# Kernel tuning notes

Hardware: AMD Instinct MI355X
Metric: run time of the kernel (lower is better)

Reference implementation:

```python
import jax, jax.numpy as jnp
import numpy as np
from jax import lax

B, H, V, T = 64, 1024, 16384, 64


def setup_inputs() -> dict:
    key = jax.random.key(0)
    ks = jax.random.split(key, 8)
    s = 1.0 / np.sqrt(H)
    return {
        "encoder_hidden": jax.random.normal(ks[0], (B, H), jnp.float32),
        "encoder_cell": jax.random.normal(ks[1], (B, H), jnp.float32),
        "W_ih": jax.random.normal(ks[2], (4 * H, H), jnp.float32) * s,
        "W_hh": jax.random.normal(ks[3], (4 * H, H), jnp.float32) * s,
        "b_ih": jnp.zeros((4 * H,), jnp.float32),
        "b_hh": jnp.zeros((4 * H,), jnp.float32),
        "W_out": jax.random.normal(ks[4], (V, H), jnp.float32) * s,
        "b_out": jnp.zeros((V,), jnp.float32),
        "embedding": jax.random.normal(ks[5], (V, H), jnp.float32),
        "init_input": jnp.zeros((1, H), jnp.float32),
        "max_len": T,
        "eos_idx": 0,
    }


def reference(encoder_hidden, encoder_cell, W_ih, W_hh, b_ih, b_hh,
              W_out, b_out, embedding, init_input, max_len, eos_idx):
    batch, hidden = encoder_hidden.shape
    vocab = W_out.shape[0]
    x0 = jnp.broadcast_to(init_input, (batch, hidden))
    mask0 = jnp.ones((1, batch), dtype=encoder_hidden.dtype)

    def step(carry, _):
        h, c, x, mask = carry
        # torch.nn.LSTMCell gate math
        gates = x @ W_ih.T + b_ih + h @ W_hh.T + b_hh  # [B, 4H]
        i, f, g, o = jnp.split(gates, 4, axis=-1)
        i = jax.nn.sigmoid(i)
        f = jax.nn.sigmoid(f)
        g = jnp.tanh(g)
        o = jax.nn.sigmoid(o)
        c_new = f * c + i * g
        h_new = o * jnp.tanh(c_new)
        logit = h_new @ W_out.T + b_out  # [B, V]
        # eval-mode path: hard argmax one-hot
        predict = jax.nn.one_hot(jnp.argmax(logit, axis=1), vocab, dtype=mask.dtype)
        mask_new = mask * (1.0 - predict[:, eos_idx])  # [1, B]
        x_next = predict @ embedding  # [B, H]
        return (h_new, c_new, x_next, mask_new), (predict, logit, mask)

    carry0 = (encoder_hidden, encoder_cell, x0, mask0)
    _, (predicts, logits, masks) = lax.scan(step, carry0, None, length=max_len)
    # predicts/logits: [T, B, V]; masks: [T, 1, B]
    return predicts, logits, masks
```

## Files before the change

### kernel.cpp

```cpp
#include <hip/hip_runtime.h>
#include <math.h>

#define B 64
#define H 1024
#define V 16384
#define T 64
constexpr int KT = 32;
constexpr size_t TBV = (size_t)T * B * V;

__global__ __launch_bounds__(256) void k_init(
    const float* __restrict__ enc_h, const float* __restrict__ enc_c,
    const float* __restrict__ init_input,
    float* __restrict__ h, float* __restrict__ c,
    float* __restrict__ x, float* __restrict__ mask)
{
    int i = blockIdx.x * 256 + threadIdx.x;
    if (i < B * H) {
        h[i] = enc_h[i];
        c[i] = enc_c[i];
        x[i] = init_input[i & (H - 1)];
    }
    if (i < B) mask[i] = 1.0f;
}

__global__ __launch_bounds__(256) void k_gates(
    const float* __restrict__ x, const float* __restrict__ h,
    const float* __restrict__ W_ih, const float* __restrict__ W_hh,
    float* __restrict__ gpart)
{
    const int nt   = blockIdx.x >> 3;
    const int ks   = blockIdx.x & 7;
    const int pair = ks >> 2;
    const int kbase = (ks & 3) * 256;
    const float* __restrict__ A = pair ? h : x;
    const float* __restrict__ W = pair ? W_hh : W_ih;

    __shared__ __align__(16) float a_lds[KT][68];
    __shared__ __align__(16) float w_lds[KT][68];

    const int tid = threadIdx.x;
    const int tb = tid >> 4;
    const int tn = tid & 15;
    float acc[4][4];
#pragma unroll
    for (int i = 0; i < 4; ++i)
#pragma unroll
        for (int j = 0; j < 4; ++j) acc[i][j] = 0.f;

    const int kk = tid & 31;
    const int r  = tid >> 5;

    for (int kc = 0; kc < 256 / KT; ++kc) {
        const int k0 = kbase + kc * KT;
#pragma unroll
        for (int j = 0; j < 8; ++j) {
            int row = r * 8 + j;
            a_lds[kk][row] = A[row * H + k0 + kk];
            w_lds[kk][row] = W[(nt * 64 + row) * H + k0 + kk];
        }
        __syncthreads();
#pragma unroll
        for (int k2 = 0; k2 < KT; ++k2) {
            float4 av = *(const float4*)&a_lds[k2][tb * 4];
            float4 wv = *(const float4*)&w_lds[k2][tn * 4];
            acc[0][0] = fmaf(av.x, wv.x, acc[0][0]);
            acc[0][1] = fmaf(av.x, wv.y, acc[0][1]);
            acc[0][2] = fmaf(av.x, wv.z, acc[0][2]);
            acc[0][3] = fmaf(av.x, wv.w, acc[0][3]);
            acc[1][0] = fmaf(av.y, wv.x, acc[1][0]);
            acc[1][1] = fmaf(av.y, wv.y, acc[1][1]);
            acc[1][2] = fmaf(av.y, wv.z, acc[1][2]);
            acc[1][3] = fmaf(av.y, wv.w, acc[1][3]);
            acc[2][0] = fmaf(av.z, wv.x, acc[2][0]);
            acc[2][1] = fmaf(av.z, wv.y, acc[2][1]);
            acc[2][2] = fmaf(av.z, wv.z, acc[2][2]);
            acc[2][3] = fmaf(av.z, wv.w, acc[2][3]);
            acc[3][0] = fmaf(av.w, wv.x, acc[3][0]);
            acc[3][1] = fmaf(av.w, wv.y, acc[3][1]);
            acc[3][2] = fmaf(av.w, wv.z, acc[3][2]);
            acc[3][3] = fmaf(av.w, wv.w, acc[3][3]);
        }
        __syncthreads();
    }

    float* outp = gpart + (size_t)ks * B * 4096;
#pragma unroll
    for (int i = 0; i < 4; ++i) {
        float4 v = make_float4(acc[i][0], acc[i][1], acc[i][2], acc[i][3]);
        *(float4*)&outp[(size_t)(tb * 4 + i) * 4096 + nt * 64 + tn * 4] = v;
    }
}

__global__ __launch_bounds__(256) void k_lstm(
    const float* __restrict__ gpart,
    const float* __restrict__ b_ih, const float* __restrict__ b_hh,
    float* __restrict__ h, float* __restrict__ c)
{
    int idx = blockIdx.x * 256 + threadIdx.x;
    int b = idx >> 10, j = idx & 1023;
    float s[4];
#pragma unroll
    for (int g = 0; g < 4; ++g) {
        int m = g * H + j;
        float v = b_ih[m] + b_hh[m];
#pragma unroll
        for (int ksp = 0; ksp < 8; ++ksp)
            v += gpart[(size_t)ksp * B * 4096 + (size_t)b * 4096 + m];
        s[g] = v;
    }
    float ig = 1.f / (1.f + expf(-s[0]));
    float fg = 1.f / (1.f + expf(-s[1]));
    float gg = tanhf(s[2]);
    float og = 1.f / (1.f + expf(-s[3]));
    float cn = fg * c[idx] + ig * gg;
    float hn = og * tanhf(cn);
    c[idx] = cn;
    h[idx] = hn;
}

__global__ __launch_bounds__(256) void k_logits(
    const float* __restrict__ h, const float* __restrict__ W_out,
    float* __restrict__ out0, float* __restrict__ lpart)
{
    const int nt = blockIdx.x >> 1;
    const int ks = blockIdx.x & 1;
    const int kbase = ks * 512;
    float* __restrict__ dst = ks ? lpart : out0;

    __shared__ __align__(16) float a_lds[KT][68];
    __shared__ __align__(16) float w_lds[KT][68];

    const int tid = threadIdx.x;
    const int tb = tid >> 4;
    const int tn = tid & 15;
    float acc[4][4];
#pragma unroll
    for (int i = 0; i < 4; ++i)
#pragma unroll
        for (int j = 0; j < 4; ++j) acc[i][j] = 0.f;

    const int kk = tid & 31;
    const int r  = tid >> 5;

    for (int kc = 0; kc < 512 / KT; ++kc) {
        const int k0 = kbase + kc * KT;
#pragma unroll
        for (int j = 0; j < 8; ++j) {
            int row = r * 8 + j;
            a_lds[kk][row] = h[row * H + k0 + kk];
            w_lds[kk][row] = W_out[(size_t)(nt * 64 + row) * H + k0 + kk];
        }
        __syncthreads();
#pragma unroll
        for (int k2 = 0; k2 < KT; ++k2) {
            float4 av = *(const float4*)&a_lds[k2][tb * 4];
            float4 wv = *(const float4*)&w_lds[k2][tn * 4];
            acc[0][0] = fmaf(av.x, wv.x, acc[0][0]);
            acc[0][1] = fmaf(av.x, wv.y, acc[0][1]);
            acc[0][2] = fmaf(av.x, wv.z, acc[0][2]);
            acc[0][3] = fmaf(av.x, wv.w, acc[0][3]);
            acc[1][0] = fmaf(av.y, wv.x, acc[1][0]);
            acc[1][1] = fmaf(av.y, wv.y, acc[1][1]);
            acc[1][2] = fmaf(av.y, wv.z, acc[1][2]);
            acc[1][3] = fmaf(av.y, wv.w, acc[1][3]);
            acc[2][0] = fmaf(av.z, wv.x, acc[2][0]);
            acc[2][1] = fmaf(av.z, wv.y, acc[2][1]);
            acc[2][2] = fmaf(av.z, wv.z, acc[2][2]);
            acc[2][3] = fmaf(av.z, wv.w, acc[2][3]);
            acc[3][0] = fmaf(av.w, wv.x, acc[3][0]);
            acc[3][1] = fmaf(av.w, wv.y, acc[3][1]);
            acc[3][2] = fmaf(av.w, wv.z, acc[3][2]);
            acc[3][3] = fmaf(av.w, wv.w, acc[3][3]);
        }
        __syncthreads();
    }

#pragma unroll
    for (int i = 0; i < 4; ++i) {
        float4 v = make_float4(acc[i][0], acc[i][1], acc[i][2], acc[i][3]);
        *(float4*)&dst[(size_t)(tb * 4 + i) * V + nt * 64 + tn * 4] = v;
    }
}

__global__ __launch_bounds__(256) void k_argmax(
    float* __restrict__ logit_t,
    const float* __restrict__ lpart,
    const float* __restrict__ b_out,
    const float* __restrict__ embedding,
    const int* __restrict__ eos_ptr,
    float* __restrict__ mask,
    float* __restrict__ x,
    float* __restrict__ predicts_t,
    float* __restrict__ masks_t)
{
    const int b = blockIdx.x, tid = threadIdx.x;
    __shared__ float sval[256];
    __shared__ int   sidx[256];

    float best = -INFINITY;
    int bi = 0;
    for (int v = tid; v < V; v += 256) {
        size_t off = (size_t)b * V + v;
        float val = logit_t[off] + lpart[off] + b_out[v];
        logit_t[off] = val;
        if (val > best) { best = val; bi = v; }
    }
    sval[tid] = best; sidx[tid] = bi;
    __syncthreads();
    for (int s = 128; s > 0; s >>= 1) {
        if (tid < s) {
            float v2 = sval[tid + s]; int i2 = sidx[tid + s];
            if (v2 > sval[tid] || (v2 == sval[tid] && i2 < sidx[tid])) {
                sval[tid] = v2; sidx[tid] = i2;
            }
        }
        __syncthreads();
    }
    int idx = sidx[0];
    if (tid == 0) {
        predicts_t[(size_t)b * V + idx] = 1.0f;
        float mb = mask[b];
        masks_t[b] = mb;
        if (idx == *eos_ptr) mask[b] = 0.0f;
    }
    const float4* emb4 = (const float4*)(embedding + (size_t)idx * H);
    float4* x4 = (float4*)(x + (size_t)b * H);
    for (int k = tid; k < H / 4; k += 256) x4[k] = emb4[k];
}

extern "C" void kernel_launch(void* const* d_in, const int* in_sizes, int n_in,
                              void* d_out, int out_size, void* d_ws, size_t ws_size,
                              hipStream_t stream)
{
    (void)in_sizes; (void)n_in; (void)out_size; (void)ws_size;

    const float* enc_h = (const float*)d_in[0];
    const float* enc_c = (const float*)d_in[1];
    const float* W_ih  = (const float*)d_in[2];
    const float* W_hh  = (const float*)d_in[3];
    const float* b_ih  = (const float*)d_in[4];
    const float* b_hh  = (const float*)d_in[5];
    const float* W_out = (const float*)d_in[6];
    const float* b_out = (const float*)d_in[7];
    const float* emb   = (const float*)d_in[8];
    const float* init_input = (const float*)d_in[9];
    const int* eos_ptr = (const int*)d_in[11];

    float* out = (float*)d_out;
    float* ws  = (float*)d_ws;
    float* h     = ws;
    float* c     = h + B * H;
    float* x     = c + B * H;
    float* mask  = x + B * H;
    float* gpart = mask + 64;
    float* lpart = gpart + 8 * B * 4096;

    hipMemsetAsync(d_out, 0, TBV * sizeof(float), stream);
    k_init<<<256, 256, 0, stream>>>(enc_h, enc_c, init_input, h, c, x, mask);

    for (int t = 0; t < T; ++t) {
        float* predicts_t = out + (size_t)t * B * V;
        float* logits_t   = out + TBV + (size_t)t * B * V;
        float* masks_t    = out + 2 * TBV + (size_t)t * B;

        k_gates<<<512, 256, 0, stream>>>(x, h, W_ih, W_hh, gpart);
        k_lstm<<<256, 256, 0, stream>>>(gpart, b_ih, b_hh, h, c);
        k_logits<<<512, 256, 0, stream>>>(h, W_out, logits_t, lpart);
        k_argmax<<<64, 256, 0, stream>>>(logits_t, lpart, b_out, emb, eos_ptr,
                                         mask, x, predicts_t, masks_t);
    }
}
```

Measured before the change: 5.254 ms.

## Use split-bf16 MFMA GEMMs for gates and logits with packed activations

Replaces the scalar FP32 FMA GEMMs for the LSTM gates and output logits with bf16 MFMA 32x32x16 kernels. Precision is kept near FP32 by splitting each operand into hi and lo bf16 parts and accumulating three products. Activations h and x are stored pre-split in a k-blocked layout so the MFMA A fragments load directly, while weights are converted on the fly into double-buffered LDS. The gates split-K drops from 8 partials to 2, which leaves only 64 blocks in that launch. The hi/lo split may still perturb argmax ties.

```diff
diff --git a/kernel.cpp b/kernel.cpp
--- a/kernel.cpp
+++ b/kernel.cpp
@@ -5,108 +5,141 @@
 #define H 1024
 #define V 16384
 #define T 64
-constexpr int KT = 32;
 constexpr size_t TBV = (size_t)T * B * V;
 
-__global__ __launch_bounds__(256) void k_init(
-    const float* __restrict__ enc_h, const float* __restrict__ enc_c,
-    const float* __restrict__ init_input,
-    float* __restrict__ h, float* __restrict__ c,
-    float* __restrict__ x, float* __restrict__ mask)
-{
-    int i = blockIdx.x * 256 + threadIdx.x;
-    if (i < B * H) {
-        h[i] = enc_h[i];
-        c[i] = enc_c[i];
-        x[i] = init_input[i & (H - 1)];
-    }
-    if (i < B) mask[i] = 1.0f;
-}
-
-__global__ __launch_bounds__(256) void k_gates(
-    const float* __restrict__ x, const float* __restrict__ h,
+typedef __attribute__((ext_vector_type(8))) short bhalf8;
+typedef __attribute__((ext_vector_type(16))) float f32x16;
+
+__device__ __forceinline__ void split_trunc(float a, unsigned short& hi, unsigned short& lo) {
+    unsigned u = __float_as_uint(a);
+    hi = (unsigned short)(u >> 16);
+    float hif = __uint_as_float(u & 0xFFFF0000u);
+    lo = (unsigned short)(__float_as_uint(a - hif) >> 16);
+}
+
+__device__ __forceinline__ void cvt8(const float* f, int4& hv, int4& lv) {
+    unsigned h[8], l[8];
+#pragma unroll
+    for (int j = 0; j < 8; ++j) {
+        unsigned u = __float_as_uint(f[j]);
+        h[j] = u >> 16;
+        float hif = __uint_as_float(u & 0xFFFF0000u);
+        l[j] = __float_as_uint(f[j] - hif) >> 16;
+    }
+    hv = make_int4((int)(h[0] | (h[1] << 16)), (int)(h[2] | (h[3] << 16)),
+                   (int)(h[4] | (h[5] << 16)), (int)(h[6] | (h[7] << 16)));
+    lv = make_int4((int)(l[0] | (l[1] << 16)), (int)(l[2] | (l[3] << 16)),
+                   (int)(l[4] | (l[5] << 16)), (int)(l[6] | (l[7] << 16)));
+}
+
+__device__ __forceinline__ void gemm_body(
+    const unsigned short* __restrict__ Ahi, const unsigned short* __restrict__ Alo,
+    const float* __restrict__ W, int k0, int nChunks,
+    float* __restrict__ dst, size_t dstride, int n0,
+    short (&sBh)[2][128][72], short (&sBl)[2][128][72])
+{
+    const int tid  = threadIdx.x;
+    const int wave = tid >> 6;
+    const int lane = tid & 63;
+    const int lrow = lane & 31;
+    const int lhalf = lane >> 5;
+
+    f32x16 acc0, acc1;
+#pragma unroll
+    for (int i = 0; i < 16; ++i) { acc0[i] = 0.f; acc1[i] = 0.f; }
+
+    const int r  = tid >> 1;
+    const int kh = (tid & 1) * 32;
+
+    {
+        const float* wr = W + (size_t)(n0 + r) * H + k0 + kh;
+        float f[32];
+#pragma unroll
+        for (int i = 0; i < 32; i += 4) *(float4*)&f[i] = *(const float4*)&wr[i];
+#pragma unroll
+        for (int i = 0; i < 32; i += 8) {
+            int4 hv, lv; cvt8(&f[i], hv, lv);
+            *(int4*)&sBh[0][r][kh + i] = hv;
+            *(int4*)&sBl[0][r][kh + i] = lv;
+        }
+    }
+    __syncthreads();
+
+    for (int c = 0; c < nChunks; ++c) {
+        const int buf = c & 1;
+        float pf[32];
+        const bool pre = (c + 1 < nChunks);
+        if (pre) {
+            const float* wr = W + (size_t)(n0 + r) * H + k0 + (c + 1) * 64 + kh;
+#pragma unroll
+            for (int i = 0; i < 32; i += 4) *(float4*)&pf[i] = *(const float4*)&wr[i];
+        }
+        const int kgb = ((k0 + c * 64) >> 3) + lhalf;
+#pragma unroll
+        for (int kt = 0; kt < 4; ++kt) {
+            const bhalf8 bh = *(const bhalf8*)&sBh[buf][wave * 32 + lrow][kt * 16 + lhalf * 8];
+            const bhalf8 bl = *(const bhalf8*)&sBl[buf][wave * 32 + lrow][kt * 16 + lhalf * 8];
+            const size_t aoff = (size_t)(kgb + kt * 2) * 512 + (size_t)lrow * 8;
+            const bhalf8 ah0 = *(const bhalf8*)(Ahi + aoff);
+            const bhalf8 al0 = *(const bhalf8*)(Alo + aoff);
+            const bhalf8 ah1 = *(const bhalf8*)(Ahi + aoff + 256);
+            const bhalf8 al1 = *(const bhalf8*)(Alo + aoff + 256);
+            acc0 = __builtin_amdgcn_mfma_f32_32x32x16_bf16(ah0, bh, acc0, 0, 0, 0);
+            acc0 = __builtin_amdgcn_mfma_f32_32x32x16_bf16(ah0, bl, acc0, 0, 0, 0);
+            acc0 = __builtin_amdgcn_mfma_f32_32x32x16_bf16(al0, bh, acc0, 0, 0, 0);
+            acc1 = __builtin_amdgcn_mfma_f32_32x32x16_bf16(ah1, bh, acc1, 0, 0, 0);
+            acc1 = __builtin_amdgcn_mfma_f32_32x32x16_bf16(ah1, bl, acc1, 0, 0, 0);
+            acc1 = __builtin_amdgcn_mfma_f32_32x32x16_bf16(al1, bh, acc1, 0, 0, 0);
+        }
+        if (pre) {
+#pragma unroll
+            for (int i = 0; i < 32; i += 8) {
+                int4 hv, lv; cvt8(&pf[i], hv, lv);
+                *(int4*)&sBh[buf ^ 1][r][kh + i] = hv;
+                *(int4*)&sBl[buf ^ 1][r][kh + i] = lv;
+            }
+        }
+        __syncthreads();
+    }
+
+    const int n = n0 + wave * 32 + lrow;
+#pragma unroll
+    for (int reg = 0; reg < 16; ++reg) {
+        int row = (reg & 3) + 8 * (reg >> 2) + 4 * lhalf;
+        dst[(size_t)row * dstride + n]        = acc0[reg];
+        dst[(size_t)(row + 32) * dstride + n] = acc1[reg];
+    }
+}
+
+__global__ __launch_bounds__(256, 2) void k_gates(
+    const unsigned short* __restrict__ xh, const unsigned short* __restrict__ xl,
+    const unsigned short* __restrict__ hh, const unsigned short* __restrict__ hl,
     const float* __restrict__ W_ih, const float* __restrict__ W_hh,
     float* __restrict__ gpart)
 {
-    const int nt   = blockIdx.x >> 3;
-    const int ks   = blockIdx.x & 7;
-    const int pair = ks >> 2;
-    const int kbase = (ks & 3) * 256;
-    const float* __restrict__ A = pair ? h : x;
-    const float* __restrict__ W = pair ? W_hh : W_ih;
-
-    __shared__ __align__(16) float a_lds[KT][68];
-    __shared__ __align__(16) float w_lds[KT][68];
-
-    const int tid = threadIdx.x;
-    const int tb = tid >> 4;
-    const int tn = tid & 15;
-    float acc[4][4];
-#pragma unroll
-    for (int i = 0; i < 4; ++i)
-#pragma unroll
-        for (int j = 0; j < 4; ++j) acc[i][j] = 0.f;
-
-    const int kk = tid & 31;
-    const int r  = tid >> 5;
-
-    for (int kc = 0; kc < 256 / KT; ++kc) {
-        const int k0 = kbase + kc * KT;
-#pragma unroll
-        for (int j = 0; j < 8; ++j) {
-            int row = r * 8 + j;
-            a_lds[kk][row] = A[row * H + k0 + kk];
-            w_lds[kk][row] = W[(nt * 64 + row) * H + k0 + kk];
-        }
-        __syncthreads();
-#pragma unroll
-        for (int k2 = 0; k2 < KT; ++k2) {
-            float4 av = *(const float4*)&a_lds[k2][tb * 4];
-            float4 wv = *(const float4*)&w_lds[k2][tn * 4];
-            acc[0][0] = fmaf(av.x, wv.x, acc[0][0]);
-            acc[0][1] = fmaf(av.x, wv.y, acc[0][1]);
-            acc[0][2] = fmaf(av.x, wv.z, acc[0][2]);
-            acc[0][3] = fmaf(av.x, wv.w, acc[0][3]);
-            acc[1][0] = fmaf(av.y, wv.x, acc[1][0]);
-            acc[1][1] = fmaf(av.y, wv.y, acc[1][1]);
-            acc[1][2] = fmaf(av.y, wv.z, acc[1][2]);
-            acc[1][3] = fmaf(av.y, wv.w, acc[1][3]);
-            acc[2][0] = fmaf(av.z, wv.x, acc[2][0]);
-            acc[2][1] = fmaf(av.z, wv.y, acc[2][1]);
-            acc[2][2] = fmaf(av.z, wv.z, acc[2][2]);
-            acc[2][3] = fmaf(av.z, wv.w, acc[2][3]);
-            acc[3][0] = fmaf(av.w, wv.x, acc[3][0]);
-            acc[3][1] = fmaf(av.w, wv.y, acc[3][1]);
-            acc[3][2] = fmaf(av.w, wv.z, acc[3][2]);
-            acc[3][3] = fmaf(av.w, wv.w, acc[3][3]);
-        }
-        __syncthreads();
-    }
-
-    float* outp = gpart + (size_t)ks * B * 4096;
-#pragma unroll
-    for (int i = 0; i < 4; ++i) {
-        float4 v = make_float4(acc[i][0], acc[i][1], acc[i][2], acc[i][3]);
-        *(float4*)&outp[(size_t)(tb * 4 + i) * 4096 + nt * 64 + tn * 4] = v;
-    }
+    __shared__ short sBh[2][128][72];
+    __shared__ short sBl[2][128][72];
+    const int nt = blockIdx.x >> 1, ks = blockIdx.x & 1;
+    if (ks == 0)
+        gemm_body(xh, xl, W_ih, 0, 16, gpart, 4096, nt * 128, sBh, sBl);
+    else
+        gemm_body(hh, hl, W_hh, 0, 16, gpart + (size_t)B * 4096, 4096, nt * 128, sBh, sBl);
 }
 
 __global__ __launch_bounds__(256) void k_lstm(
     const float* __restrict__ gpart,
     const float* __restrict__ b_ih, const float* __restrict__ b_hh,
-    float* __restrict__ h, float* __restrict__ c)
+    float* __restrict__ c,
+    unsigned short* __restrict__ hh, unsigned short* __restrict__ hl)
 {
     int idx = blockIdx.x * 256 + threadIdx.x;
     int b = idx >> 10, j = idx & 1023;
     float s[4];
 #pragma unroll
     for (int g = 0; g < 4; ++g) {
-        int m = g * H + j;
-        float v = b_ih[m] + b_hh[m];
-#pragma unroll
-        for (int ksp = 0; ksp < 8; ++ksp)
-            v += gpart[(size_t)ksp * B * 4096 + (size_t)b * 4096 + m];
-        s[g] = v;
+        int m = g * 1024 + j;
+        s[g] = b_ih[m] + b_hh[m] + gpart[(size_t)b * 4096 + m]
+             + gpart[(size_t)(B + b) * 4096 + m];
     }
     float ig = 1.f / (1.f + expf(-s[0]));
     float fg = 1.f / (1.f + expf(-s[1]));
@@ -115,83 +148,27 @@
     float cn = fg * c[idx] + ig * gg;
     float hn = og * tanhf(cn);
     c[idx] = cn;
-    h[idx] = hn;
-}
-
-__global__ __launch_bounds__(256) void k_logits(
-    const float* __restrict__ h, const float* __restrict__ W_out,
-    float* __restrict__ out0, float* __restrict__ lpart)
-{
-    const int nt = blockIdx.x >> 1;
-    const int ks = blockIdx.x & 1;
-    const int kbase = ks * 512;
-    float* __restrict__ dst = ks ? lpart : out0;
-
-    __shared__ __align__(16) float a_lds[KT][68];
-    __shared__ __align__(16) float w_lds[KT][68];
-
-    const int tid = threadIdx.x;
-    const int tb = tid >> 4;
-    const int tn = tid & 15;
-    float acc[4][4];
-#pragma unroll
-    for (int i = 0; i < 4; ++i)
-#pragma unroll
-        for (int j = 0; j < 4; ++j) acc[i][j] = 0.f;
-
-    const int kk = tid & 31;
-    const int r  = tid >> 5;
-
-    for (int kc = 0; kc < 512 / KT; ++kc) {
-        const int k0 = kbase + kc * KT;
-#pragma unroll
-        for (int j = 0; j < 8; ++j) {
-            int row = r * 8 + j;
-            a_lds[kk][row] = h[row * H + k0 + kk];
-            w_lds[kk][row] = W_out[(size_t)(nt * 64 + row) * H + k0 + kk];
-        }
-        __syncthreads();
-#pragma unroll
-        for (int k2 = 0; k2 < KT; ++k2) {
-            float4 av = *(const float4*)&a_lds[k2][tb * 4];
-            float4 wv = *(const float4*)&w_lds[k2][tn * 4];
-            acc[0][0] = fmaf(av.x, wv.x, acc[0][0]);
-            acc[0][1] = fmaf(av.x, wv.y, acc[0][1]);
-            acc[0][2] = fmaf(av.x, wv.z, acc[0][2]);
-            acc[0][3] = fmaf(av.x, wv.w, acc[0][3]);
-            acc[1][0] = fmaf(av.y, wv.x, acc[1][0]);
-            acc[1][1] = fmaf(av.y, wv.y, acc[1][1]);
-            acc[1][2] = fmaf(av.y, wv.z, acc[1][2]);
-            acc[1][3] = fmaf(av.y, wv.w, acc[1][3]);
-            acc[2][0] = fmaf(av.z, wv.x, acc[2][0]);
-            acc[2][1] = fmaf(av.z, wv.y, acc[2][1]);
-            acc[2][2] = fmaf(av.z, wv.z, acc[2][2]);
-            acc[2][3] = fmaf(av.z, wv.w, acc[2][3]);
-            acc[3][0] = fmaf(av.w, wv.x, acc[3][0]);
-            acc[3][1] = fmaf(av.w, wv.y, acc[3][1]);
-            acc[3][2] = fmaf(av.w, wv.z, acc[3][2]);
-            acc[3][3] = fmaf(av.w, wv.w, acc[3][3]);
-        }
-        __syncthreads();
-    }
-
-#pragma unroll
-    for (int i = 0; i < 4; ++i) {
-        float4 v = make_float4(acc[i][0], acc[i][1], acc[i][2], acc[i][3]);
-        *(float4*)&dst[(size_t)(tb * 4 + i) * V + nt * 64 + tn * 4] = v;
-    }
+    unsigned short hi, lo; split_trunc(hn, hi, lo);
+    size_t fo = (size_t)(j >> 3) * 512 + (size_t)b * 8 + (j & 7);
+    hh[fo] = hi; hl[fo] = lo;
+}
+
+__global__ __launch_bounds__(256, 2) void k_logits(
+    const unsigned short* __restrict__ hh, const unsigned short* __restrict__ hl,
+    const float* __restrict__ W_out, float* __restrict__ out0, float* __restrict__ lpart)
+{
+    __shared__ short sBh[2][128][72];
+    __shared__ short sBl[2][128][72];
+    const int nt = blockIdx.x >> 1, ks = blockIdx.x & 1;
+    gemm_body(hh, hl, W_out, ks * 512, 8, ks ? lpart : out0, V, nt * 128, sBh, sBl);
 }
 
 __global__ __launch_bounds__(256) void k_argmax(
-    float* __restrict__ logit_t,
-    const float* __restrict__ lpart,
-    const float* __restrict__ b_out,
-    const float* __restrict__ embedding,
-    const int* __restrict__ eos_ptr,
-    float* __restrict__ mask,
-    float* __restrict__ x,
-    float* __restrict__ predicts_t,
-    float* __restrict__ masks_t)
+    float* __restrict__ logit_t, const float* __restrict__ lpart,
+    const float* __restrict__ b_out, const float* __restrict__ embedding,
+    const int* __restrict__ eos_ptr, float* __restrict__ mask,
+    unsigned short* __restrict__ xh, unsigned short* __restrict__ xl,
+    float* __restrict__ predicts_t, float* __restrict__ masks_t)
 {
     const int b = blockIdx.x, tid = threadIdx.x;
     __shared__ float sval[256];
@@ -223,9 +200,31 @@
         masks_t[b] = mb;
         if (idx == *eos_ptr) mask[b] = 0.0f;
     }
-    const float4* emb4 = (const float4*)(embedding + (size_t)idx * H);
-    float4* x4 = (float4*)(x + (size_t)b * H);
-    for (int k = tid; k < H / 4; k += 256) x4[k] = emb4[k];
+    for (int k = tid; k < H; k += 256) {
+        unsigned short hi, lo; split_trunc(embedding[(size_t)idx * H + k], hi, lo);
+        size_t fo = (size_t)(k >> 3) * 512 + (size_t)b * 8 + (k & 7);
+        xh[fo] = hi; xl[fo] = lo;
+    }
+}
+
+__global__ __launch_bounds__(256) void k_init(
+    const float* __restrict__ enc_h, const float* __restrict__ enc_c,
+    const float* __restrict__ init_input,
+    float* __restrict__ c,
+    unsigned short* __restrict__ hh, unsigned short* __restrict__ hl,
+    unsigned short* __restrict__ xh, unsigned short* __restrict__ xl,
+    float* __restrict__ mask)
+{
+    int i = blockIdx.x * 256 + threadIdx.x;
+    int b = i >> 10, j = i & 1023;
+    c[i] = enc_c[i];
+    unsigned short hi, lo;
+    split_trunc(enc_h[i], hi, lo);
+    size_t fo = (size_t)(j >> 3) * 512 + (size_t)b * 8 + (j & 7);
+    hh[fo] = hi; hl[fo] = lo;
+    split_trunc(init_input[j], hi, lo);
+    xh[fo] = hi; xl[fo] = lo;
+    if (i < B) mask[i] = 1.0f;
 }
 
 extern "C" void kernel_launch(void* const* d_in, const int* in_sizes, int n_in,
@@ -248,25 +247,27 @@
 
     float* out = (float*)d_out;
     float* ws  = (float*)d_ws;
-    float* h     = ws;
-    float* c     = h + B * H;
-    float* x     = c + B * H;
-    float* mask  = x + B * H;
+    float* c     = ws;
+    float* mask  = c + 65536;
     float* gpart = mask + 64;
-    float* lpart = gpart + 8 * B * 4096;
+    float* lpart = gpart + 524288;
+    unsigned short* xh = (unsigned short*)(lpart + 1048576);
+    unsigned short* xl = xh + 65536;
+    unsigned short* hh = xl + 65536;
+    unsigned short* hl = hh + 65536;
 
     hipMemsetAsync(d_out, 0, TBV * sizeof(float), stream);
-    k_init<<<256, 256, 0, stream>>>(enc_h, enc_c, init_input, h, c, x, mask);
+    k_init<<<256, 256, 0, stream>>>(enc_h, enc_c, init_input, c, hh, hl, xh, xl, mask);
 
     for (int t = 0; t < T; ++t) {
         float* predicts_t = out + (size_t)t * B * V;
         float* logits_t   = out + TBV + (size_t)t * B * V;
         float* masks_t    = out + 2 * TBV + (size_t)t * B;
 
-        k_gates<<<512, 256, 0, stream>>>(x, h, W_ih, W_hh, gpart);
-        k_lstm<<<256, 256, 0, stream>>>(gpart, b_ih, b_hh, h, c);
-        k_logits<<<512, 256, 0, stream>>>(h, W_out, logits_t, lpart);
+        k_gates<<<64, 256, 0, stream>>>(xh, xl, hh, hl, W_ih, W_hh, gpart);
+        k_lstm<<<256, 256, 0, stream>>>(gpart, b_ih, b_hh, c, hh, hl);
+        k_logits<<<256, 256, 0, stream>>>(hh, hl, W_out, logits_t, lpart);
         k_argmax<<<64, 256, 0, stream>>>(logits_t, lpart, b_out, emb, eos_ptr,
-                                         mask, x, predicts_t, masks_t);
-    }
-}
+                                         mask, xh, xl, predicts_t, masks_t);
+    }
+}
```

After: 5.266 ms. Within noise of the previous version (+0.2%).
